# Optimization experiments

Hardware: AMD Instinct MI355X
Metric: run time of the kernel (lower is better)

## Reference

```python
import jax, jax.numpy as jnp
import numpy as np

N_NODES = 8192
HIDDEN = 256
HEADS = 4
HEAD_DIM = HIDDEN // HEADS
NUM_EDGES = 4096
NUM_INC = 65536
LN_EPS = 1e-5


def setup_inputs() -> dict:
    key = jax.random.key(0)
    ks = jax.random.split(key, 8)
    scale = HIDDEN ** -0.5
    return {
        "x": jax.random.normal(ks[0], (N_NODES, HIDDEN), jnp.float32),
        "node_idx": jax.random.randint(ks[1], (NUM_INC,), 0, N_NODES),
        "edge_idx": jax.random.randint(ks[2], (NUM_INC,), 0, NUM_EDGES),
        "W_w": jax.random.normal(ks[3], (HIDDEN, HIDDEN), jnp.float32) * scale,
        "W_b": jax.random.normal(ks[4], (HIDDEN,), jnp.float32) * 0.02,
        "edge_att": jax.random.normal(ks[5], (HEADS, HEAD_DIM), jnp.float32) * scale,
        "out_w": jax.random.normal(ks[6], (HIDDEN, HIDDEN), jnp.float32) * scale,
        "out_b": jax.random.normal(ks[7], (HIDDEN,), jnp.float32) * 0.02,
    }


def reference(x, node_idx, edge_idx, W_w, W_b, edge_att, out_w, out_b):
    n = x.shape[0]
    e = node_idx.shape[0]
    # x' = W(x), split into heads: [N, heads, head_dim]
    xw = (x @ W_w.T + W_b).reshape(n, HEADS, HEAD_DIM)
    feat = xw[node_idx]                                   # [E, heads, hd]
    logits = jnp.einsum("ehd,hd->eh", feat, edge_att)      # [E, heads]
    # segment softmax over nodes within each hyperedge, per head
    seg_max = jax.ops.segment_max(logits, edge_idx, num_segments=NUM_EDGES)
    p = jnp.exp(logits - seg_max[edge_idx])
    seg_sum = jax.ops.segment_sum(p, edge_idx, num_segments=NUM_EDGES)
    attn = p / seg_sum[edge_idx]                           # [E, heads]
    attn_mean = attn.mean(axis=1)                          # mean over heads, [E]
    # hyperedges with < 2 nodes are skipped in the original
    sizes = jax.ops.segment_sum(jnp.ones((e,), x.dtype), edge_idx, num_segments=NUM_EDGES)
    valid = sizes[edge_idx] >= 2.0
    attn_mean = jnp.where(valid, attn_mean, 0.0)
    # scatter-add attention-weighted ORIGINAL features back to nodes
    contrib = attn_mean[:, None] * x[node_idx]             # [E, H]
    out = jnp.zeros_like(x).at[node_idx].add(contrib)
    # degree normalization counts ALL incidences (including size-1 edges)
    counts = jnp.zeros((n,), x.dtype).at[node_idx].add(1.0)
    out = out / jnp.clip(counts, 1.0)[:, None]
    out = out @ out_w.T + out_b
    # fresh nn.LayerNorm => affine identity, biased variance, eps=1e-5
    mu = out.mean(-1, keepdims=True)
    var = ((out - mu) ** 2).mean(-1, keepdims=True)
    out = (out - mu) / jnp.sqrt(var + LN_EPS)
    # NxN pairwise attention accumulation: AW[i,j] = sum_e attn_i(e)*count_j(e), diag zeroed
    A = jnp.zeros((n, NUM_EDGES), x.dtype).at[node_idx, edge_idx].add(attn_mean)
    B = jnp.zeros((n, NUM_EDGES), x.dtype).at[node_idx, edge_idx].add(1.0)
    attention_weights = A @ B.T
    attention_weights = attention_weights.at[jnp.diag_indices(n)].set(0.0)
    return out, attention_weights
```

## Files before the change

kernel.cpp:

```cpp
#include <hip/hip_runtime.h>
#include <stdint.h>

#define N_NODES  8192
#define HIDDEN   256
#define HEADS    4
#define HEAD_DIM 64
#define NUM_EDGES 4096
#define NUM_INC  65536
#define LN_EPS   1e-5f

typedef unsigned int uint_t;
typedef float __attribute__((ext_vector_type(4))) f4v;


#define OFF_SEGSZ    0
#define OFF_NCNT     16384
#define OFF_NFILL    49152
#define OFF_EFILL    81920
#define ZERO_BYTES   98304
#define OFF_VKH      98304
#define OFF_BL       102400
#define OFF_LOGIT    102464
#define OFF_NPTR     233536
#define OFF_EPTR     266320
#define OFF_SEGSUM   282720
#define OFF_NINC     348256
#define OFF_EMEM     610400
#define OFF_ITEM     872544

__global__ __launch_bounds__(256) void k_foldzero(const float* __restrict__ Ww,
                                                  const float* __restrict__ Wb,
                                                  const float* __restrict__ ea,
                                                  float* __restrict__ vkhT,
                                                  float* __restrict__ bl,
                                                  uint_t* __restrict__ zw) {
    int t = threadIdx.x, b = blockIdx.x;
    zw[b * 256 + t] = 0u;
    if (b < HEADS) {
        int k = t, h = b;
        float a = 0.f;
        for (int d = 0; d < HEAD_DIM; ++d)
            a += ea[h * HEAD_DIM + d] * Ww[(size_t)(h * HEAD_DIM + d) * HIDDEN + k];
        vkhT[h * HIDDEN + k] = a;
        if (k == 0) {
            float s = 0.f;
            for (int d = 0; d < HEAD_DIM; ++d)
                s += Wb[h * HEAD_DIM + d] * ea[h * HEAD_DIM + d];
            bl[h] = s;
        }
    }
}

__global__ __launch_bounds__(256) void k_logits(const float* __restrict__ x,
                                                const float* __restrict__ vkhT,
                                                const float* __restrict__ bl,
                                                const int* __restrict__ node_idx,
                                                const int* __restrict__ edge_idx,
                                                int* __restrict__ seg_size,
                                                int* __restrict__ node_cnt,
                                                float* __restrict__ logit) {
    __shared__ __align__(16) float xs[32 * HIDDEN];
    __shared__ __align__(16) float vs[HEADS * HIDDEN];
    __shared__ float bls[HEADS];
    int t = threadIdx.x, b = blockIdx.x;
    {
        int i = b * 256 + t;
        atomicAdd(&seg_size[edge_idx[i]], 1);
        atomicAdd(&node_cnt[node_idx[i]], 1);
    }
    float4* xsv = (float4*)xs;
    const float4* xg = (const float4*)(x + (size_t)b * 32 * HIDDEN);
    #pragma unroll
    for (int i = 0; i < 8; ++i) xsv[i * 256 + t] = xg[i * 256 + t];
    ((float4*)vs)[t] = ((const float4*)vkhT)[t];
    if (t < HEADS) bls[t] = bl[t];
    __syncthreads();
    if (t < 128) {
        int n = t >> 2, h = t & 3;
        const float4* xr = (const float4*)(xs + n * HIDDEN);
        const float4* vr = (const float4*)(vs + h * HIDDEN);
        float acc = bls[h];
        for (int k4 = 0; k4 < HIDDEN / 4; ++k4) {
            float4 xv = xr[k4], vv = vr[k4];
            acc += xv.x * vv.x + xv.y * vv.y + xv.z * vv.z + xv.w * vv.w;
        }
        logit[(b * 32 + n) * HEADS + h] = acc;
    }
}

__global__ __launch_bounds__(256) void k_scan(const int* __restrict__ node_cnt, int* __restrict__ node_ptr,
                                              const int* __restrict__ seg_size, int* __restrict__ edge_ptr) {
    __shared__ int part[256];
    const int* cnt; int* ptr; int n;
    if (blockIdx.x == 0) { cnt = node_cnt; ptr = node_ptr; n = N_NODES; }
    else                 { cnt = seg_size; ptr = edge_ptr; n = NUM_EDGES; }
    int t = threadIdx.x, C = n / 256;
    int s = 0;
    for (int j = 0; j < C; ++j) s += cnt[t * C + j];
    part[t] = s;
    __syncthreads();
    if (t == 0) {
        int run = 0;
        for (int i = 0; i < 256; ++i) { int tmp = part[i]; part[i] = run; run += tmp; }
        ptr[n] = run;
    }
    __syncthreads();
    int run = part[t];
    for (int j = 0; j < C; ++j) { ptr[t * C + j] = run; run += cnt[t * C + j]; }
}

__global__ void k_fill(const int* __restrict__ node_idx, const int* __restrict__ edge_idx,
                       const int* __restrict__ node_ptr, const int* __restrict__ edge_ptr,
                       int* __restrict__ node_fill, int* __restrict__ edge_fill,
                       int* __restrict__ node_inc, int* __restrict__ edge_mem) {
    int i = blockIdx.x * 256 + threadIdx.x;
    int n = node_idx[i], e = edge_idx[i];
    int p = node_ptr[n] + atomicAdd(&node_fill[n], 1);
    node_inc[p] = i;
    int q = edge_ptr[e] + atomicAdd(&edge_fill[e], 1);
    edge_mem[q] = n;
}

__global__ __launch_bounds__(256) void k_seg(const int* __restrict__ edge_ptr,
                                             const int* __restrict__ edge_mem,
                                             const float* __restrict__ logit,
                                             float* __restrict__ seg_sum) {
    int e = blockIdx.x * 256 + threadIdx.x;
    int qb = edge_ptr[e], qe = edge_ptr[e + 1];
    float s0 = 0, s1 = 0, s2 = 0, s3 = 0;
    for (int q = qb; q < qe; ++q) {
        int j = edge_mem[q];
        s0 += __expf(logit[j * 4 + 0]);
        s1 += __expf(logit[j * 4 + 1]);
        s2 += __expf(logit[j * 4 + 2]);
        s3 += __expf(logit[j * 4 + 3]);
    }
    seg_sum[e * 4 + 0] = s0; seg_sum[e * 4 + 1] = s1;
    seg_sum[e * 4 + 2] = s2; seg_sum[e * 4 + 3] = s3;
}

__global__ __launch_bounds__(256) void k_pairs(const int* __restrict__ node_inc,
                                               const int* __restrict__ node_idx,
                                               const int* __restrict__ edge_idx,
                                               const int* __restrict__ edge_ptr,
                                               const float* __restrict__ logit,
                                               const float* __restrict__ seg_sum,
                                               float4* __restrict__ item) {
    int p = blockIdx.x * 256 + threadIdx.x;
    int m = node_inc[p];
    int e = edge_idx[m];
    int qb = edge_ptr[e], qe = edge_ptr[e + 1];
    float a = 0.f;
    if (qe - qb >= 2) {
        int n = node_idx[m];
        float s = 0.f;
        #pragma unroll
        for (int h = 0; h < HEADS; ++h)
            s += __expf(logit[n * HEADS + h]) / seg_sum[e * HEADS + h];
        a = 0.25f * s;
    }
    float4 it;
    it.x = a;
    it.y = __int_as_float(qb);
    it.z = __int_as_float(qe);
    it.w = 0.f;
    item[p] = it;
}

__global__ __launch_bounds__(256) void k_aw_out(const float4* __restrict__ item,
                                                const int* __restrict__ node_ptr,
                                                const int* __restrict__ edge_mem,
                                                const float* __restrict__ x,
                                                const float* __restrict__ out_w,
                                                const float* __restrict__ out_b,
                                                float* __restrict__ AW,
                                                float* __restrict__ out0) {
    __shared__ __align__(16) float buf[N_NODES];
    __shared__ float sr[16], mu_s[16], rs_s[16];
    int t = threadIdx.x, w = t >> 6, lane = t & 63;
    int b = blockIdx.x;

    if (b >= 512) {
        int i = b - 512;
        int pb = node_ptr[i], pe = node_ptr[i + 1];
        int p0 = pb + w;
        float4 nxt = (p0 < pe) ? item[p0] : make_float4(0.f, 0.f, 0.f, 0.f);
        float4* rowv = (float4*)buf;
        #pragma unroll
        for (int c = 0; c < 8; ++c) rowv[c * 256 + t] = make_float4(0.f, 0.f, 0.f, 0.f);
        __syncthreads();
        for (int p = p0; p < pe; p += 4) {
            float4 it = nxt;
            if (p + 4 < pe) nxt = item[p + 4];
            float a = it.x;
            if (a != 0.f) {
                int qb = __float_as_int(it.y), qe = __float_as_int(it.z);
                for (int q = qb + lane; q < qe; q += 64)
                    atomicAdd(&buf[edge_mem[q]], a);
            }
        }
        __syncthreads();
        if (t == 0) buf[i] = 0.f;
        __syncthreads();
        f4v* dst = (f4v*)(AW + (size_t)i * N_NODES);
        #pragma unroll
        for (int c = 0; c < 8; ++c)
            __builtin_nontemporal_store(((const f4v*)rowv)[c * 256 + t], &dst[c * 256 + t]);
        return;
    }

    float (*y)[260] = (float (*)[260])buf;
    int R = b * 16;
    if (t < 16) {
        int n = R + t;
        int nb = node_ptr[n], ne = node_ptr[n + 1];
        float ws = 0.f;
        for (int p = nb; p < ne; ++p) ws += item[p].x;
        int c = ne - nb; if (c < 1) c = 1;
        sr[t] = ws / (float)c;
    }
    __syncthreads();
    #pragma unroll
    for (int r = 0; r < 16; ++r)
        y[r][t] = sr[r] * x[(size_t)(R + r) * HIDDEN + t];
    __syncthreads();
    float acc[16];
    float bias = out_b[t];
    #pragma unroll
    for (int r = 0; r < 16; ++r) acc[r] = bias;
    const float4* wr4 = (const float4*)(out_w + (size_t)t * HIDDEN);
    for (int j4 = 0; j4 < HIDDEN / 4; ++j4) {
        float4 wv = wr4[j4];
        #pragma unroll
        for (int r = 0; r < 16; ++r) {
            float4 yv = *(const float4*)&y[r][j4 * 4];
            acc[r] += yv.x * wv.x + yv.y * wv.y + yv.z * wv.z + yv.w * wv.w;
        }
    }
    __syncthreads();
    #pragma unroll
    for (int r = 0; r < 16; ++r) y[r][t] = acc[r];
    __syncthreads();
    #pragma unroll
    for (int rr = 0; rr < 4; ++rr) {
        int r = (w << 2) | rr;
        float v = y[r][lane] + y[r][lane + 64] + y[r][lane + 128] + y[r][lane + 192];
        #pragma unroll
        for (int off = 32; off; off >>= 1) v += __shfl_down(v, off, 64);
        float mu = __shfl(v, 0, 64) * (1.0f / HIDDEN);
        float d0 = y[r][lane] - mu, d1 = y[r][lane + 64] - mu;
        float d2 = y[r][lane + 128] - mu, d3 = y[r][lane + 192] - mu;
        float s2 = d0 * d0 + d1 * d1 + d2 * d2 + d3 * d3;
        #pragma unroll
        for (int off = 32; off; off >>= 1) s2 += __shfl_down(s2, off, 64);
        if (lane == 0) {
            mu_s[r] = mu;
            rs_s[r] = rsqrtf(s2 * (1.0f / HIDDEN) + LN_EPS);
        }
    }
    __syncthreads();
    #pragma unroll
    for (int r = 0; r < 16; ++r)
        out0[(size_t)(R + r) * HIDDEN + t] = (y[r][t] - mu_s[r]) * rs_s[r];
}

extern "C" void kernel_launch(void* const* d_in, const int* in_sizes, int n_in,
                              void* d_out, int out_size, void* d_ws, size_t ws_size,
                              hipStream_t stream) {
    const float* x        = (const float*)d_in[0];
    const int*   node_idx = (const int*)d_in[1];
    const int*   edge_idx = (const int*)d_in[2];
    const float* Ww       = (const float*)d_in[3];
    const float* Wb       = (const float*)d_in[4];
    const float* ea       = (const float*)d_in[5];
    const float* ow       = (const float*)d_in[6];
    const float* ob       = (const float*)d_in[7];
    float* out0 = (float*)d_out;
    float* aw   = out0 + (size_t)N_NODES * HIDDEN;

    char* ws = (char*)d_ws;
    int*    seg_size  = (int*)(ws + OFF_SEGSZ);
    int*    node_cnt  = (int*)(ws + OFF_NCNT);
    int*    node_fill = (int*)(ws + OFF_NFILL);
    int*    edge_fill = (int*)(ws + OFF_EFILL);
    float*  vkhT      = (float*)(ws + OFF_VKH);
    float*  bl        = (float*)(ws + OFF_BL);
    float*  logit     = (float*)(ws + OFF_LOGIT);
    int*    node_ptr  = (int*)(ws + OFF_NPTR);
    int*    edge_ptr  = (int*)(ws + OFF_EPTR);
    float*  seg_sum   = (float*)(ws + OFF_SEGSUM);
    int*    node_inc  = (int*)(ws + OFF_NINC);
    int*    edge_mem  = (int*)(ws + OFF_EMEM);
    float4* item      = (float4*)(ws + OFF_ITEM);

    k_foldzero<<<ZERO_BYTES / 4 / 256, 256, 0, stream>>>(Ww, Wb, ea, vkhT, bl, (uint_t*)ws);
    k_logits<<<N_NODES / 32, 256, 0, stream>>>(x, vkhT, bl, node_idx, edge_idx,
                                               seg_size, node_cnt, logit);
    k_scan<<<2, 256, 0, stream>>>(node_cnt, node_ptr, seg_size, edge_ptr);
    k_fill<<<NUM_INC / 256, 256, 0, stream>>>(node_idx, edge_idx, node_ptr, edge_ptr,
                                              node_fill, edge_fill, node_inc, edge_mem);
    k_seg<<<NUM_EDGES / 256, 256, 0, stream>>>(edge_ptr, edge_mem, logit, seg_sum);
    k_pairs<<<NUM_INC / 256, 256, 0, stream>>>(node_inc, node_idx, edge_idx, edge_ptr,
                                               logit, seg_sum, item);
    k_aw_out<<<N_NODES + 512, 256, 0, stream>>>(item, node_ptr, edge_mem, x, ow, ob, aw, out0);
}
```

Baseline: 361.4 us.

## Fuse segment-sum into fill and recompute attention inline, removing two kernels

Segment exp-sums are now accumulated with float atomics inside the fill kernel, which removes the separate per-edge reduction kernel. The per-incidence item buffer and its kernel are gone too: the final kernel recomputes each attention weight from logits and segment sums as it walks node incidences, and the per-node weight sum is now split over 16 lanes with a shuffle reduction. This saves two launches and the item buffer round trip, at the cost of atomic contention on segment sums, extra dependent gathers (node_inc→edge_idx→edge_ptr) in the hot loop, and float atomics whose accumulation order varies between runs.

```diff
diff --git a/kernel.cpp b/kernel.cpp
--- a/kernel.cpp
+++ b/kernel.cpp
@@ -17,16 +17,15 @@
 #define OFF_NCNT     16384
 #define OFF_NFILL    49152
 #define OFF_EFILL    81920
-#define ZERO_BYTES   98304
-#define OFF_VKH      98304
-#define OFF_BL       102400
-#define OFF_LOGIT    102464
-#define OFF_NPTR     233536
-#define OFF_EPTR     266320
-#define OFF_SEGSUM   282720
-#define OFF_NINC     348256
-#define OFF_EMEM     610400
-#define OFF_ITEM     872544
+#define OFF_SEGSUM   98304
+#define ZERO_BYTES   163840
+#define OFF_VKH      163840
+#define OFF_BL       167936
+#define OFF_LOGIT    168192
+#define OFF_NPTR     299264
+#define OFF_EPTR     332288
+#define OFF_NINC     348928
+#define OFF_EMEM     611072
 
 __global__ __launch_bounds__(256) void k_foldzero(const float* __restrict__ Ww,
                                                   const float* __restrict__ Wb,
@@ -112,64 +111,28 @@
 __global__ void k_fill(const int* __restrict__ node_idx, const int* __restrict__ edge_idx,
                        const int* __restrict__ node_ptr, const int* __restrict__ edge_ptr,
                        int* __restrict__ node_fill, int* __restrict__ edge_fill,
-                       int* __restrict__ node_inc, int* __restrict__ edge_mem) {
+                       int* __restrict__ node_inc, int* __restrict__ edge_mem,
+                       const float* __restrict__ logit, float* __restrict__ seg_sum) {
     int i = blockIdx.x * 256 + threadIdx.x;
     int n = node_idx[i], e = edge_idx[i];
     int p = node_ptr[n] + atomicAdd(&node_fill[n], 1);
     node_inc[p] = i;
     int q = edge_ptr[e] + atomicAdd(&edge_fill[e], 1);
     edge_mem[q] = n;
-}
-
-__global__ __launch_bounds__(256) void k_seg(const int* __restrict__ edge_ptr,
-                                             const int* __restrict__ edge_mem,
-                                             const float* __restrict__ logit,
-                                             float* __restrict__ seg_sum) {
-    int e = blockIdx.x * 256 + threadIdx.x;
-    int qb = edge_ptr[e], qe = edge_ptr[e + 1];
-    float s0 = 0, s1 = 0, s2 = 0, s3 = 0;
-    for (int q = qb; q < qe; ++q) {
-        int j = edge_mem[q];
-        s0 += __expf(logit[j * 4 + 0]);
-        s1 += __expf(logit[j * 4 + 1]);
-        s2 += __expf(logit[j * 4 + 2]);
-        s3 += __expf(logit[j * 4 + 3]);
-    }
-    seg_sum[e * 4 + 0] = s0; seg_sum[e * 4 + 1] = s1;
-    seg_sum[e * 4 + 2] = s2; seg_sum[e * 4 + 3] = s3;
-}
-
-__global__ __launch_bounds__(256) void k_pairs(const int* __restrict__ node_inc,
-                                               const int* __restrict__ node_idx,
-                                               const int* __restrict__ edge_idx,
-                                               const int* __restrict__ edge_ptr,
-                                               const float* __restrict__ logit,
-                                               const float* __restrict__ seg_sum,
-                                               float4* __restrict__ item) {
-    int p = blockIdx.x * 256 + threadIdx.x;
-    int m = node_inc[p];
-    int e = edge_idx[m];
-    int qb = edge_ptr[e], qe = edge_ptr[e + 1];
-    float a = 0.f;
-    if (qe - qb >= 2) {
-        int n = node_idx[m];
-        float s = 0.f;
-        #pragma unroll
-        for (int h = 0; h < HEADS; ++h)
-            s += __expf(logit[n * HEADS + h]) / seg_sum[e * HEADS + h];
-        a = 0.25f * s;
-    }
-    float4 it;
-    it.x = a;
-    it.y = __int_as_float(qb);
-    it.z = __int_as_float(qe);
-    it.w = 0.f;
-    item[p] = it;
-}
-
-__global__ __launch_bounds__(256) void k_aw_out(const float4* __restrict__ item,
-                                                const int* __restrict__ node_ptr,
+    const float4 lg = *(const float4*)(logit + (size_t)n * 4);
+    atomicAdd(&seg_sum[e * 4 + 0], __expf(lg.x));
+    atomicAdd(&seg_sum[e * 4 + 1], __expf(lg.y));
+    atomicAdd(&seg_sum[e * 4 + 2], __expf(lg.z));
+    atomicAdd(&seg_sum[e * 4 + 3], __expf(lg.w));
+}
+
+__global__ __launch_bounds__(256) void k_aw_out(const int* __restrict__ node_ptr,
+                                                const int* __restrict__ node_inc,
+                                                const int* __restrict__ edge_idx,
+                                                const int* __restrict__ edge_ptr,
                                                 const int* __restrict__ edge_mem,
+                                                const float* __restrict__ logit,
+                                                const float* __restrict__ seg_sum,
                                                 const float* __restrict__ x,
                                                 const float* __restrict__ out_w,
                                                 const float* __restrict__ out_b,
@@ -183,18 +146,23 @@
     if (b >= 512) {
         int i = b - 512;
         int pb = node_ptr[i], pe = node_ptr[i + 1];
-        int p0 = pb + w;
-        float4 nxt = (p0 < pe) ? item[p0] : make_float4(0.f, 0.f, 0.f, 0.f);
+        const float4 lg = *(const float4*)(logit + (size_t)i * 4);
+        float ex0 = __expf(lg.x), ex1 = __expf(lg.y);
+        float ex2 = __expf(lg.z), ex3 = __expf(lg.w);
         float4* rowv = (float4*)buf;
         #pragma unroll
         for (int c = 0; c < 8; ++c) rowv[c * 256 + t] = make_float4(0.f, 0.f, 0.f, 0.f);
+        int p = pb + w;
+        int m_nxt = (p < pe) ? node_inc[p] : 0;
         __syncthreads();
-        for (int p = p0; p < pe; p += 4) {
-            float4 it = nxt;
-            if (p + 4 < pe) nxt = item[p + 4];
-            float a = it.x;
-            if (a != 0.f) {
-                int qb = __float_as_int(it.y), qe = __float_as_int(it.z);
+        for (; p < pe; p += 4) {
+            int m = m_nxt;
+            if (p + 4 < pe) m_nxt = node_inc[p + 4];
+            int e = edge_idx[m];
+            int qb = edge_ptr[e], qe = edge_ptr[e + 1];
+            if (qe - qb >= 2) {
+                const float4 ss = *(const float4*)(seg_sum + (size_t)e * 4);
+                float a = 0.25f * (ex0 / ss.x + ex1 / ss.y + ex2 / ss.z + ex3 / ss.w);
                 for (int q = qb + lane; q < qe; q += 64)
                     atomicAdd(&buf[edge_mem[q]], a);
             }
@@ -211,13 +179,29 @@
 
     float (*y)[260] = (float (*)[260])buf;
     int R = b * 16;
-    if (t < 16) {
-        int n = R + t;
+    {
+        int nl = t >> 4, s = t & 15;
+        int n = R + nl;
         int nb = node_ptr[n], ne = node_ptr[n + 1];
-        float ws = 0.f;
-        for (int p = nb; p < ne; ++p) ws += item[p].x;
-        int c = ne - nb; if (c < 1) c = 1;
-        sr[t] = ws / (float)c;
+        const float4 lg = *(const float4*)(logit + (size_t)n * 4);
+        float ex0 = __expf(lg.x), ex1 = __expf(lg.y);
+        float ex2 = __expf(lg.z), ex3 = __expf(lg.w);
+        float wsum = 0.f;
+        for (int p = nb + s; p < ne; p += 16) {
+            int m = node_inc[p];
+            int e = edge_idx[m];
+            int qb = edge_ptr[e], qe = edge_ptr[e + 1];
+            if (qe - qb >= 2) {
+                const float4 ss = *(const float4*)(seg_sum + (size_t)e * 4);
+                wsum += 0.25f * (ex0 / ss.x + ex1 / ss.y + ex2 / ss.z + ex3 / ss.w);
+            }
+        }
+        #pragma unroll
+        for (int off = 1; off < 16; off <<= 1) wsum += __shfl_xor(wsum, off, 64);
+        if (s == 0) {
+            int c = ne - nb; if (c < 1) c = 1;
+            sr[nl] = wsum / (float)c;
+        }
     }
     __syncthreads();
     #pragma unroll
@@ -283,24 +267,22 @@
     int*    node_cnt  = (int*)(ws + OFF_NCNT);
     int*    node_fill = (int*)(ws + OFF_NFILL);
     int*    edge_fill = (int*)(ws + OFF_EFILL);
+    float*  seg_sum   = (float*)(ws + OFF_SEGSUM);
     float*  vkhT      = (float*)(ws + OFF_VKH);
     float*  bl        = (float*)(ws + OFF_BL);
     float*  logit     = (float*)(ws + OFF_LOGIT);
     int*    node_ptr  = (int*)(ws + OFF_NPTR);
     int*    edge_ptr  = (int*)(ws + OFF_EPTR);
-    float*  seg_sum   = (float*)(ws + OFF_SEGSUM);
     int*    node_inc  = (int*)(ws + OFF_NINC);
     int*    edge_mem  = (int*)(ws + OFF_EMEM);
-    float4* item      = (float4*)(ws + OFF_ITEM);
 
     k_foldzero<<<ZERO_BYTES / 4 / 256, 256, 0, stream>>>(Ww, Wb, ea, vkhT, bl, (uint_t*)ws);
     k_logits<<<N_NODES / 32, 256, 0, stream>>>(x, vkhT, bl, node_idx, edge_idx,
                                                seg_size, node_cnt, logit);
     k_scan<<<2, 256, 0, stream>>>(node_cnt, node_ptr, seg_size, edge_ptr);
     k_fill<<<NUM_INC / 256, 256, 0, stream>>>(node_idx, edge_idx, node_ptr, edge_ptr,
-                                              node_fill, edge_fill, node_inc, edge_mem);
-    k_seg<<<NUM_EDGES / 256, 256, 0, stream>>>(edge_ptr, edge_mem, logit, seg_sum);
-    k_pairs<<<NUM_INC / 256, 256, 0, stream>>>(node_inc, node_idx, edge_idx, edge_ptr,
-                                               logit, seg_sum, item);
-    k_aw_out<<<N_NODES + 512, 256, 0, stream>>>(item, node_ptr, edge_mem, x, ow, ob, aw, out0);
-}
+                                              node_fill, edge_fill, node_inc, edge_mem,
+                                              logit, seg_sum);
+    k_aw_out<<<N_NODES + 512, 256, 0, stream>>>(node_ptr, node_inc, edge_idx, edge_ptr,
+                                                edge_mem, logit, seg_sum, x, ow, ob, aw, out0);
+}
```

Result: no change. 368.3 us (+1.9%).
